# Performance work log

Hardware: AMD Instinct MI355X
Metric: run time of the kernel (lower is better)

Reference implementation:

```python
import jax, jax.numpy as jnp
import numpy as np

N = 100000   # nodes
E = 1600000  # edges (avg degree 16)
IDIM = 128
HDIM = 128   # heads=1, so heads*hdim == hdim
ODIM = 40
L = 4        # num_layers


def setup_inputs() -> dict:
    key = jax.random.key(0)
    ks = jax.random.split(key, 12)
    s = 0.05  # init scale
    inp = {
        "x": jax.random.normal(ks[0], (N, IDIM), jnp.float32),
        "edge_index": jax.random.randint(ks[1], (2, E), 0, N, jnp.int32),
        # input projection (idim -> hdim)
        "lin_W": jax.random.normal(ks[2], (IDIM, HDIM), jnp.float32) * s,
        "lin_b": jnp.zeros((HDIM,), jnp.float32),
        # stacked per-layer transformer-conv weights (heads=1)
        "Wq": jax.random.normal(ks[3], (L, HDIM, HDIM), jnp.float32) * s,
        "bq": jnp.zeros((L, HDIM), jnp.float32),
        "Wk": jax.random.normal(ks[4], (L, HDIM, HDIM), jnp.float32) * s,
        "bk": jnp.zeros((L, HDIM), jnp.float32),
        "Wv": jax.random.normal(ks[5], (L, HDIM, HDIM), jnp.float32) * s,
        "bv": jnp.zeros((L, HDIM), jnp.float32),
        "Ws": jax.random.normal(ks[6], (L, HDIM, HDIM), jnp.float32) * s,  # lin_skip
        "bs": jnp.zeros((L, HDIM), jnp.float32),
        # output classifier (hdim -> odim)
        "fc_W": jax.random.normal(ks[7], (HDIM, ODIM), jnp.float32) * s,
        "fc_b": jnp.zeros((ODIM,), jnp.float32),
    }
    return inp


def reference(x, edge_index, lin_W, lin_b, Wq, bq, Wk, bk, Wv, bv, Ws, bs, fc_W, fc_b):
    src = edge_index[0]  # x_j (message source)
    dst = edge_index[1]  # x_i (aggregation target / softmax segment)
    scale = 1.0 / np.sqrt(HDIM).astype(np.float32)

    h = x @ lin_W + lin_b  # [N, HDIM]
    for l in range(L):
        q = h @ Wq[l] + bq[l]  # [N, C]
        k = h @ Wk[l] + bk[l]
        v = h @ Wv[l] + bv[l]
        # per-edge attention logits: (W3 x_i) . (W4 x_j) / sqrt(d)
        logits = jnp.sum(q[dst] * k[src], axis=-1) * scale  # [E]
        # segment softmax over incoming edges of each dst node
        m = jax.ops.segment_max(logits, dst, num_segments=N)
        m = jnp.where(jnp.isfinite(m), m, 0.0)  # guard isolated nodes
        e = jnp.exp(logits - m[dst])
        den = jax.ops.segment_sum(e, dst, num_segments=N)
        alpha = e / jnp.where(den > 0, den, 1.0)[dst]  # [E]
        # weighted scatter-add aggregation
        agg = jax.ops.segment_sum(alpha[:, None] * v[src], dst, num_segments=N)  # [N, C]
        # root/skip connection (root_weight=True, beta=False)
        h = agg + (h @ Ws[l] + bs[l])
        if l < L - 1:
            h = jax.nn.elu(h)
    return jax.nn.log_softmax(h @ fc_W + fc_b, axis=1)  # [N, ODIM]
```

## Files before the change

### kernel.cpp

```cpp
#include <hip/hip_runtime.h>
#include <hip/hip_bf16.h>
#include <math.h>


#define HD 128
#define ODIM 40
#define LDSA 136
#define QK_SCALE_L2E 0.1275174368437563f
#define FIXED_M 8.0f

#define BKT_CAP 8192

typedef __attribute__((ext_vector_type(8))) short short8;
typedef __attribute__((ext_vector_type(4))) float f4v;
typedef __attribute__((ext_vector_type(2))) float f2v;
typedef __attribute__((ext_vector_type(4))) unsigned short us4;
typedef __attribute__((ext_vector_type(8))) unsigned short us8;
typedef __attribute__((ext_vector_type(4))) int i4v;
typedef long long ll64;

static __device__ __forceinline__ float b2f(unsigned short u) {
  return __uint_as_float(((unsigned)u) << 16);
}
static __device__ __forceinline__ unsigned short f2b(float f) {
  __hip_bfloat16 h = __float2bfloat16(f);
  return __builtin_bit_cast(unsigned short, h);
}


__global__ __launch_bounds__(256) void k_zero(int* __restrict__ p, int n) {
  int i = blockIdx.x * 256 + threadIdx.x;
  if (i < n) p[i] = 0;
}

__global__ __launch_bounds__(256) void k_bin(const int* __restrict__ src, const int* __restrict__ dst,
                                             int E, int NB, int* __restrict__ bucket_wp,
                                             unsigned int* __restrict__ staged) {
  __shared__ int cnt[512];
  __shared__ int lbase[512];
  int t = threadIdx.x;
  int e0 = blockIdx.x * 8192;
  for (int b = t; b < NB; b += 256) cnt[b] = 0;
  __syncthreads();
#pragma unroll
  for (int i = 0; i < 32; ++i) {
    int e = e0 + i * 256 + t;
    if (e < E) atomicAdd(&cnt[dst[e] >> 8], 1);
  }
  __syncthreads();
  for (int b = t; b < NB; b += 256) {
    int c = cnt[b];
    lbase[b] = (c > 0) ? atomicAdd(&bucket_wp[b], c) : 0;
    cnt[b] = 0;
  }
  __syncthreads();
#pragma unroll
  for (int i = 0; i < 32; ++i) {
    int e = e0 + i * 256 + t;
    if (e < E) {
      int d = dst[e];
      int b = d >> 8;
      int off = atomicAdd(&cnt[b], 1);
      int idx = lbase[b] + off;
      if (idx < BKT_CAP) {
        unsigned rec = (unsigned)src[e] | ((unsigned)(d & 255) << 17);
        staged[(size_t)b * BKT_CAP + idx] = rec;
      }
    }
  }
}

__global__ __launch_bounds__(512) void k_bscan(const int* __restrict__ bucket_wp, int NB, int E, int N,
                                               int* __restrict__ bucket_base, int* __restrict__ rowptr) {
  __shared__ int buf[512];
  int t = threadIdx.x;
  int v = (t < NB) ? bucket_wp[t] : 0;
  buf[t] = v;
  __syncthreads();
  for (int off = 1; off < 512; off <<= 1) {
    int x = (t >= off) ? buf[t - off] : 0;
    __syncthreads();
    buf[t] += x;
    __syncthreads();
  }
  if (t < NB) bucket_base[t] = buf[t] - v;
  if (t == 0) rowptr[N] = E;
}

__global__ __launch_bounds__(256) void k_csr(const unsigned int* __restrict__ staged,
                                             const int* __restrict__ bucket_wp,
                                             const int* __restrict__ bucket_base,
                                             int N, int* __restrict__ rowptr, int* __restrict__ colsrc) {
  __shared__ unsigned int srec[BKT_CAP];
  __shared__ int ncnt[256];
  __shared__ int noff[256];
  int b = blockIdx.x, t = threadIdx.x;
  int cnt = bucket_wp[b];
  if (cnt > BKT_CAP) cnt = BKT_CAP;
  int base = bucket_base[b];
  const unsigned int* gsrc = staged + (size_t)b * BKT_CAP;
  for (int i = t; i < cnt; i += 256) srec[i] = gsrc[i];
  ncnt[t] = 0;
  __syncthreads();
  for (int i = t; i < cnt; i += 256) atomicAdd(&ncnt[srec[i] >> 17], 1);
  __syncthreads();
  int v = ncnt[t];
  noff[t] = v;
  __syncthreads();
  for (int off = 1; off < 256; off <<= 1) {
    int x = (t >= off) ? noff[t - off] : 0;
    __syncthreads();
    noff[t] += x;
    __syncthreads();
  }
  int excl = noff[t] - v;
  int node = (b << 8) + t;
  if (node < N) rowptr[node] = base + excl;
  ncnt[t] = excl;
  __syncthreads();
  for (int i = t; i < cnt; i += 256) {
    unsigned rec = srec[i];
    int dl = rec >> 17;
    int pos = atomicAdd(&ncnt[dl], 1);
    colsrc[base + pos] = (int)(rec & 0x1FFFFu);
  }
}


#define PACK_FC   278528
#define PACK_TOT  284672

__global__ __launch_bounds__(256) void k_pack(const float* __restrict__ linW,
                                              const float* __restrict__ Wq, const float* __restrict__ Wk,
                                              const float* __restrict__ Wv, const float* __restrict__ Ws,
                                              const float* __restrict__ fcW,
                                              unsigned short* __restrict__ Wp) {
  int idx = blockIdx.x * 256 + threadIdx.x;
  float val;
  if (idx < 16384) {
    int n = idx >> 7, kk = idx & 127;
    val = linW[kk * 128 + n];
  } else if (idx < PACK_FC) {
    int t = idx - 16384;
    int l = t >> 16, r = t & 65535;
    int n_pos = r >> 7, k_pos = r & 127;
    int which = n_pos >> 7;
    int nn = n_pos & 127;
    int kk = 16 * (k_pos & 7) + (k_pos >> 3);
    const float* W = (which == 0) ? Wq : (which == 1) ? Wk : (which == 2) ? Wv : Ws;
    val = W[(size_t)l * 16384 + kk * 128 + nn];
  } else if (idx < PACK_TOT) {
    int t = idx - PACK_FC;
    int n = t >> 7, k_pos = t & 127;
    int kk = 16 * (k_pos & 7) + (k_pos >> 3);
    val = (n < ODIM) ? fcW[kk * ODIM + n] : 0.f;
  } else {
    return;
  }
  Wp[idx] = f2b(val);
}


__global__ __launch_bounds__(256) void k_gemm_lin(const float* __restrict__ x,
                                                  const unsigned short* __restrict__ wl,
                                                  const float* __restrict__ bias,
                                                  unsigned short* __restrict__ hb, int N) {
  __shared__ unsigned short As[32 * LDSA];
  int t = threadIdx.x;
  int rowbase = blockIdx.x * 32;
#pragma unroll
  for (int i = 0; i < 2; ++i) {
    int c = t + i * 256;
    int r = c >> 4, c8 = c & 15;
    int gr = rowbase + r;
    if (gr >= N) gr = N - 1;
    const float4* xp = (const float4*)(x + (size_t)gr * 128 + c8 * 8);
    float4 u0 = xp[0], u1 = xp[1];
    us8 o;
    o[0] = f2b(u0.x); o[1] = f2b(u0.y); o[2] = f2b(u0.z); o[3] = f2b(u0.w);
    o[4] = f2b(u1.x); o[5] = f2b(u1.y); o[6] = f2b(u1.z); o[7] = f2b(u1.w);
    *(us8*)(As + r * LDSA + c8 * 8) = o;
  }
  __syncthreads();

  int lane = t & 63, w = t >> 6;
  int rh = (w & 1) * 16;
  int ch = (w >> 1) * 64;
  int lm = lane & 15, lq = lane >> 4;

  short8 a[4];
#pragma unroll
  for (int ks = 0; ks < 4; ++ks)
    a[ks] = *(const short8*)(As + (rh + lm) * LDSA + ks * 32 + lq * 8);

  f4v acc[4];
#pragma unroll
  for (int ct = 0; ct < 4; ++ct) acc[ct] = (f4v){0.f, 0.f, 0.f, 0.f};

#pragma unroll
  for (int ct = 0; ct < 4; ++ct) {
    const short8* bp = (const short8*)(wl + ((size_t)(ch + ct * 16 + lm)) * 128 + lq * 8);
    short8 b0 = bp[0], b1 = bp[4], b2 = bp[8], b3 = bp[12];
    acc[ct] = __builtin_amdgcn_mfma_f32_16x16x32_bf16(a[0], b0, acc[ct], 0, 0, 0);
    acc[ct] = __builtin_amdgcn_mfma_f32_16x16x32_bf16(a[1], b1, acc[ct], 0, 0, 0);
    acc[ct] = __builtin_amdgcn_mfma_f32_16x16x32_bf16(a[2], b2, acc[ct], 0, 0, 0);
    acc[ct] = __builtin_amdgcn_mfma_f32_16x16x32_bf16(a[3], b3, acc[ct], 0, 0, 0);
  }

  float bv[4];
#pragma unroll
  for (int ct = 0; ct < 4; ++ct) bv[ct] = bias[ch + ct * 16 + lm];

#pragma unroll
  for (int r = 0; r < 4; ++r) {
    int row = rowbase + rh + lq * 4 + r;
    if (row < N) {
      us4 ov;
#pragma unroll
      for (int ct = 0; ct < 4; ++ct) ov[ct] = f2b(acc[ct][r] + bv[ct]);
      *(us4*)(hb + (size_t)row * 128 + lm * 8 + (w >> 1) * 4) = ov;
    }
  }
}


__global__ __launch_bounds__(256, 3) void k_gemm_qkvs(const unsigned short* __restrict__ hb,
                                                      const unsigned short* __restrict__ wl,
                                                      const float* __restrict__ bq, const float* __restrict__ bk,
                                                      const float* __restrict__ bv, const float* __restrict__ bs,
                                                      unsigned char* __restrict__ q8, unsigned char* __restrict__ k8,
                                                      unsigned char* __restrict__ v8, unsigned short* __restrict__ s,
                                                      int N) {
  __shared__ unsigned short As[32 * LDSA];
  int t = threadIdx.x;
  int rowbase = blockIdx.x * 32;
#pragma unroll
  for (int i = 0; i < 2; ++i) {
    int c = t + i * 256;
    int r = c >> 4, c8 = c & 15;
    int gr = rowbase + r;
    if (gr >= N) gr = N - 1;
    *(us8*)(As + r * LDSA + c8 * 8) = *(const us8*)(hb + (size_t)gr * 128 + c8 * 8);
  }
  __syncthreads();

  int lane = t & 63, w = t >> 6;
  int lm = lane & 15, lq = lane >> 4;

  short8 a[2][4];
#pragma unroll
  for (int rt = 0; rt < 2; ++rt)
#pragma unroll
    for (int ks = 0; ks < 4; ++ks)
      a[rt][ks] = *(const short8*)(As + (rt * 16 + lm) * LDSA + ks * 32 + lq * 8);

  f4v acc[2][8];
#pragma unroll
  for (int rt = 0; rt < 2; ++rt)
#pragma unroll
    for (int ct = 0; ct < 8; ++ct) acc[rt][ct] = (f4v){0.f, 0.f, 0.f, 0.f};

  const unsigned short* wb = wl + (size_t)w * 16384;
#pragma unroll
  for (int ct = 0; ct < 8; ++ct) {
    const short8* bp = (const short8*)(wb + (size_t)(ct * 16 + lm) * 128 + lq * 8);
    short8 b0 = bp[0], b1 = bp[4], b2 = bp[8], b3 = bp[12];
#pragma unroll
    for (int rt = 0; rt < 2; ++rt) {
      acc[rt][ct] = __builtin_amdgcn_mfma_f32_16x16x32_bf16(a[rt][0], b0, acc[rt][ct], 0, 0, 0);
      acc[rt][ct] = __builtin_amdgcn_mfma_f32_16x16x32_bf16(a[rt][1], b1, acc[rt][ct], 0, 0, 0);
      acc[rt][ct] = __builtin_amdgcn_mfma_f32_16x16x32_bf16(a[rt][2], b2, acc[rt][ct], 0, 0, 0);
      acc[rt][ct] = __builtin_amdgcn_mfma_f32_16x16x32_bf16(a[rt][3], b3, acc[rt][ct], 0, 0, 0);
    }
  }

  const float* bsel = (w == 0) ? bq : (w == 1) ? bk : (w == 2) ? bv : bs;
  float bias[8];
#pragma unroll
  for (int ct = 0; ct < 8; ++ct) bias[ct] = bsel[ct * 16 + lm];

#pragma unroll
  for (int rt = 0; rt < 2; ++rt) {
#pragma unroll
    for (int r = 0; r < 4; ++r) {
      int row = rowbase + rt * 16 + lq * 4 + r;
      if (row >= N) continue;
      float vals[8];
#pragma unroll
      for (int ct = 0; ct < 8; ++ct) vals[ct] = acc[rt][ct][r] + bias[ct];
      if (w <= 2) {
        float sc = (w == 1) ? QK_SCALE_L2E : 1.0f;
        unsigned u0 = __builtin_amdgcn_cvt_pk_fp8_f32(vals[0] * sc, vals[1] * sc, 0, false);
        u0 = __builtin_amdgcn_cvt_pk_fp8_f32(vals[2] * sc, vals[3] * sc, u0, true);
        unsigned u1 = __builtin_amdgcn_cvt_pk_fp8_f32(vals[4] * sc, vals[5] * sc, 0, false);
        u1 = __builtin_amdgcn_cvt_pk_fp8_f32(vals[6] * sc, vals[7] * sc, u1, true);
        uint2 kw; kw.x = u0; kw.y = u1;
        unsigned char* outp = (w == 0) ? q8 : (w == 1) ? k8 : v8;
        *(uint2*)(outp + (size_t)row * 128 + lm * 8) = kw;
      } else {
        us8 ov;
#pragma unroll
        for (int ct = 0; ct < 8; ++ct) ov[ct] = f2b(vals[ct]);
        *(us8*)(s + (size_t)row * 128 + lm * 8) = ov;
      }
    }
  }
}


__global__ __launch_bounds__(256, 8) void k_attn_mfma(const unsigned char* __restrict__ q8,
                                                      const unsigned char* __restrict__ kb8,
                                                      const unsigned char* __restrict__ v8,
                                                      const unsigned short* __restrict__ s,
                                                      const int* __restrict__ rowptr, const int* __restrict__ colsrc,
                                                      unsigned short* __restrict__ hb, int n, int do_elu) {
  int wid = blockIdx.x * 4 + (threadIdx.x >> 6);
  if (wid >= n) return;
  int lane = threadIdx.x & 63;
  int lm = lane & 15;
  int lq = lane >> 4;

  const unsigned char* qrow = q8 + (size_t)wid * 128;
  ll64 Bf[4];
#pragma unroll
  for (int km = 0; km < 4; ++km)
    Bf[km] = *(const ll64*)(qrow + km * 32 + lq * 8);

  int e0 = rowptr[wid], e1 = rowptr[wid + 1];

  float Sp = 0.f;
  f2v av[4];
#pragma unroll
  for (int i = 0; i < 4; ++i) av[i] = (f2v){0.f, 0.f};

  for (int ebase = e0; ebase < e1; ebase += 16) {
    int ja = colsrc[min(ebase + lm, e1 - 1)];
    const unsigned char* krow = kb8 + (size_t)ja * 128;
    ll64 Af[4];
#pragma unroll
    for (int km = 0; km < 4; ++km)
      Af[km] = *(const ll64*)(krow + km * 32 + lq * 8);

    uint2 vw[4];
#pragma unroll
    for (int r = 0; r < 4; ++r) {
      int jv = __shfl(ja, lq * 4 + r, 64);
      vw[r] = *(const uint2*)(v8 + (size_t)jv * 128 + lm * 8);
    }

    f4v c = (f4v){0.f, 0.f, 0.f, 0.f};
#pragma unroll
    for (int km = 0; km < 4; ++km)
      c = __builtin_amdgcn_mfma_f32_16x16x32_fp8_fp8(Af[km], Bf[km], c, 0, 0, 0);

    float w[4];
#pragma unroll
    for (int r = 0; r < 4; ++r)
      w[r] = (ebase + lq * 4 + r < e1) ? exp2f(c[r] - FIXED_M) : 0.f;
    Sp += (w[0] + w[1]) + (w[2] + w[3]);
#pragma unroll
    for (int r = 0; r < 4; ++r) {
      f2v p01 = __builtin_amdgcn_cvt_pk_f32_fp8(vw[r].x, false);
      f2v p23 = __builtin_amdgcn_cvt_pk_f32_fp8(vw[r].x, true);
      f2v p45 = __builtin_amdgcn_cvt_pk_f32_fp8(vw[r].y, false);
      f2v p67 = __builtin_amdgcn_cvt_pk_f32_fp8(vw[r].y, true);
      f2v wv = (f2v){w[r], w[r]};
      av[0] += p01 * wv;
      av[1] += p23 * wv;
      av[2] += p45 * wv;
      av[3] += p67 * wv;
    }
  }

#pragma unroll
  for (int off = 16; off <= 32; off <<= 1) {
    Sp += __shfl_xor(Sp, off, 64);
#pragma unroll
    for (int i = 0; i < 4; ++i) {
      av[i][0] += __shfl_xor(av[i][0], off, 64);
      av[i][1] += __shfl_xor(av[i][1], off, 64);
    }
  }

  if (lq == 0) {
    int d0 = lm * 8;
    float inv = (Sp > 0.f) ? 1.f / Sp : 0.f;
    us8 sk = *(const us8*)(s + (size_t)wid * 128 + d0);
    us8 ov;
#pragma unroll
    for (int i = 0; i < 8; ++i) {
      float x = av[i / 2][i & 1] * inv + b2f(sk[i]);
      if (do_elu) x = (x > 0.f) ? x : (__expf(x) - 1.f);
      ov[i] = f2b(x);
    }
    *(us8*)(hb + (size_t)wid * 128 + d0) = ov;
  }
}


__global__ __launch_bounds__(256) void k_fc_mfma(const unsigned short* __restrict__ hb,
                                                 const unsigned short* __restrict__ fcp,
                                                 const float* __restrict__ fcb,
                                                 float* __restrict__ out, int N) {
  __shared__ unsigned short As[64 * LDSA];
  int t = threadIdx.x;
  int rowbase = blockIdx.x * 64;
#pragma unroll
  for (int i = 0; i < 4; ++i) {
    int c = t + i * 256;
    int r = c >> 4, c8 = c & 15;
    int gr = rowbase + r;
    if (gr >= N) gr = N - 1;
    us8 val = *(const us8*)(hb + (size_t)gr * 128 + c8 * 8);
    *(us8*)(As + r * LDSA + c8 * 8) = val;
  }
  __syncthreads();

  int lane = t & 63, w = t >> 6;
  int rh = w * 16;
  int lm = lane & 15, lq = lane >> 4;

  short8 a[4];
#pragma unroll
  for (int ks = 0; ks < 4; ++ks)
    a[ks] = *(const short8*)(As + (rh + lm) * LDSA + ks * 32 + lq * 8);

  f4v acc[3];
#pragma unroll
  for (int ct = 0; ct < 3; ++ct) acc[ct] = (f4v){0.f, 0.f, 0.f, 0.f};

#pragma unroll
  for (int ct = 0; ct < 3; ++ct) {
    const short8* bp = (const short8*)(fcp + ((size_t)(ct * 16 + lm)) * 128 + lq * 8);
    short8 b0 = bp[0], b1 = bp[4], b2 = bp[8], b3 = bp[12];
    acc[ct] = __builtin_amdgcn_mfma_f32_16x16x32_bf16(a[0], b0, acc[ct], 0, 0, 0);
    acc[ct] = __builtin_amdgcn_mfma_f32_16x16x32_bf16(a[1], b1, acc[ct], 0, 0, 0);
    acc[ct] = __builtin_amdgcn_mfma_f32_16x16x32_bf16(a[2], b2, acc[ct], 0, 0, 0);
    acc[ct] = __builtin_amdgcn_mfma_f32_16x16x32_bf16(a[3], b3, acc[ct], 0, 0, 0);
  }

  float bias[3];
#pragma unroll
  for (int ct = 0; ct < 3; ++ct) {
    int c = ct * 16 + lm;
    bias[ct] = (c < ODIM) ? fcb[c] : 0.f;
  }

#pragma unroll
  for (int r = 0; r < 4; ++r) {
    float v0 = acc[0][r] + bias[0];
    float v1 = acc[1][r] + bias[1];
    float v2 = (32 + lm < ODIM) ? (acc[2][r] + bias[2]) : -INFINITY;
    float m = fmaxf(fmaxf(v0, v1), v2);
#pragma unroll
    for (int off = 1; off <= 8; off <<= 1) m = fmaxf(m, __shfl_xor(m, off, 64));
    float sum = __expf(v0 - m) + __expf(v1 - m) + ((32 + lm < ODIM) ? __expf(v2 - m) : 0.f);
#pragma unroll
    for (int off = 1; off <= 8; off <<= 1) sum += __shfl_xor(sum, off, 64);
    float lse = m + logf(sum);
    int row = rowbase + rh + lq * 4 + r;
    if (row < N) {
      float* orow = out + (size_t)row * ODIM;
      orow[lm] = v0 - lse;
      orow[16 + lm] = v1 - lse;
      if (32 + lm < ODIM) orow[32 + lm] = v2 - lse;
    }
  }
}


extern "C" void kernel_launch(void* const* d_in, const int* in_sizes, int n_in,
                              void* d_out, int out_size, void* d_ws, size_t ws_size,
                              hipStream_t stream) {
  const float* x    = (const float*)d_in[0];
  const int*   ei   = (const int*)d_in[1];
  const float* linW = (const float*)d_in[2];
  const float* linb = (const float*)d_in[3];
  const float* Wq   = (const float*)d_in[4];
  const float* bq   = (const float*)d_in[5];
  const float* Wk   = (const float*)d_in[6];
  const float* bk   = (const float*)d_in[7];
  const float* Wv   = (const float*)d_in[8];
  const float* bv   = (const float*)d_in[9];
  const float* Wsk  = (const float*)d_in[10];
  const float* bsk  = (const float*)d_in[11];
  const float* fcW  = (const float*)d_in[12];
  const float* fcb  = (const float*)d_in[13];
  float* out = (float*)d_out;

  const int N = in_sizes[0] / HD;
  const int E = in_sizes[1] / 2;
  const int* srcv = ei;
  const int* dstv = ei + E;
  const int NB = (N + 255) >> 8;

  size_t off = 0;
  char* base = (char*)d_ws;
  auto carve = [&](size_t bytes) -> void* {
    void* p = base + off;
    off = (off + bytes + 255) & ~(size_t)255;
    return p;
  };
  unsigned short* Wp = (unsigned short*)carve((size_t)PACK_TOT * 2);
  unsigned short* hb = (unsigned short*)carve((size_t)N * HD * 2);
  unsigned char*  q8 = (unsigned char*)carve((size_t)N * HD);
  unsigned char*  k8 = (unsigned char*)carve((size_t)N * HD);
  unsigned char*  v8 = (unsigned char*)carve((size_t)N * HD);
  unsigned short* sbuf = (unsigned short*)carve((size_t)N * HD * 2);
  int* rowptr = (int*)carve((size_t)(N + 1) * 4);
  int* colsrc = (int*)carve((size_t)E * 4);
  int* bucket_wp   = (int*)carve((size_t)NB * 4);
  int* bucket_base = (int*)carve((size_t)NB * 4);
  unsigned int* staged = (unsigned int*)carve((size_t)NB * BKT_CAP * 4);
  (void)ws_size; (void)n_in; (void)out_size;

  dim3 blk(256);
  int gx = (N + 31) / 32;
  int wb = (N + 3) / 4;

  k_zero<<<(NB + 255) / 256, blk, 0, stream>>>(bucket_wp, NB);
  k_bin<<<(E + 8191) / 8192, blk, 0, stream>>>(srcv, dstv, E, NB, bucket_wp, staged);
  k_bscan<<<1, 512, 0, stream>>>(bucket_wp, NB, E, N, bucket_base, rowptr);
  k_csr<<<NB, blk, 0, stream>>>(staged, bucket_wp, bucket_base, N, rowptr, colsrc);

  k_pack<<<(PACK_TOT + 255) / 256, blk, 0, stream>>>(linW, Wq, Wk, Wv, Wsk, fcW, Wp);

  k_gemm_lin<<<gx, blk, 0, stream>>>(x, Wp, linb, hb, N);

  for (int l = 0; l < 4; ++l) {
    const unsigned short* wl = Wp + 16384 + (size_t)l * 65536;
    k_gemm_qkvs<<<gx, blk, 0, stream>>>(hb, wl, bq + l * HD, bk + l * HD, bv + l * HD, bsk + l * HD,
                                        q8, k8, v8, sbuf, N);
    k_attn_mfma<<<wb, blk, 0, stream>>>(q8, k8, v8, sbuf, rowptr, colsrc, hb, N, (l < 3) ? 1 : 0);
  }

  k_fc_mfma<<<(N + 63) / 64, blk, 0, stream>>>(hb, Wp + PACK_FC, fcb, out, N);
}
```

Before: 798.7 us.

## Interleave K and V rows and process 32 edges per attention iteration

K and V fp8 rows are stored interleaved in a single 256-byte-per-node buffer, so a neighbour's K and V sit in adjacent memory and gathers have better locality. The attention loop now handles two 16-edge groups per iteration, issuing twice as many independent gathers and MFMAs to hide memory latency. Occupancy hint drops from 8 to 6 blocks per CU because the unrolled loop needs more registers. Nodes with fewer than 32 edges waste some lanes on masked work.

```diff
diff --git a/kernel.cpp b/kernel.cpp
--- a/kernel.cpp
+++ b/kernel.cpp
@@ -16,7 +16,6 @@
 typedef __attribute__((ext_vector_type(2))) float f2v;
 typedef __attribute__((ext_vector_type(4))) unsigned short us4;
 typedef __attribute__((ext_vector_type(8))) unsigned short us8;
-typedef __attribute__((ext_vector_type(4))) int i4v;
 typedef long long ll64;
 
 static __device__ __forceinline__ float b2f(unsigned short u) {
@@ -228,8 +227,8 @@
                                                       const unsigned short* __restrict__ wl,
                                                       const float* __restrict__ bq, const float* __restrict__ bk,
                                                       const float* __restrict__ bv, const float* __restrict__ bs,
-                                                      unsigned char* __restrict__ q8, unsigned char* __restrict__ k8,
-                                                      unsigned char* __restrict__ v8, unsigned short* __restrict__ s,
+                                                      unsigned char* __restrict__ q8, unsigned char* __restrict__ kv,
+                                                      unsigned short* __restrict__ s,
                                                       int N) {
   __shared__ unsigned short As[32 * LDSA];
   int t = threadIdx.x;
@@ -295,8 +294,10 @@
         unsigned u1 = __builtin_amdgcn_cvt_pk_fp8_f32(vals[4] * sc, vals[5] * sc, 0, false);
         u1 = __builtin_amdgcn_cvt_pk_fp8_f32(vals[6] * sc, vals[7] * sc, u1, true);
         uint2 kw; kw.x = u0; kw.y = u1;
-        unsigned char* outp = (w == 0) ? q8 : (w == 1) ? k8 : v8;
-        *(uint2*)(outp + (size_t)row * 128 + lm * 8) = kw;
+        unsigned char* outp = (w == 0) ? (q8 + (size_t)row * 128 + lm * 8)
+                            : (w == 1) ? (kv + (size_t)row * 256 + lm * 8)
+                                       : (kv + (size_t)row * 256 + 128 + lm * 8);
+        *(uint2*)outp = kw;
       } else {
         us8 ov;
 #pragma unroll
@@ -308,9 +309,8 @@
 }
 
 
-__global__ __launch_bounds__(256, 8) void k_attn_mfma(const unsigned char* __restrict__ q8,
-                                                      const unsigned char* __restrict__ kb8,
-                                                      const unsigned char* __restrict__ v8,
+__global__ __launch_bounds__(256, 6) void k_attn_mfma(const unsigned char* __restrict__ q8,
+                                                      const unsigned char* __restrict__ kv,
                                                       const unsigned short* __restrict__ s,
                                                       const int* __restrict__ rowptr, const int* __restrict__ colsrc,
                                                       unsigned short* __restrict__ hb, int n, int do_elu) {
@@ -333,42 +333,54 @@
 #pragma unroll
   for (int i = 0; i < 4; ++i) av[i] = (f2v){0.f, 0.f};
 
-  for (int ebase = e0; ebase < e1; ebase += 16) {
-    int ja = colsrc[min(ebase + lm, e1 - 1)];
-    const unsigned char* krow = kb8 + (size_t)ja * 128;
-    ll64 Af[4];
-#pragma unroll
-    for (int km = 0; km < 4; ++km)
-      Af[km] = *(const ll64*)(krow + km * 32 + lq * 8);
-
-    uint2 vw[4];
+  for (int ebase = e0; ebase < e1; ebase += 32) {
+    int ja0 = colsrc[min(ebase + lm, e1 - 1)];
+    int ja1 = colsrc[min(ebase + 16 + lm, e1 - 1)];
+    const unsigned char* kr0 = kv + (size_t)ja0 * 256;
+    const unsigned char* kr1 = kv + (size_t)ja1 * 256;
+    ll64 Af0[4], Af1[4];
+#pragma unroll
+    for (int km = 0; km < 4; ++km) {
+      Af0[km] = *(const ll64*)(kr0 + km * 32 + lq * 8);
+      Af1[km] = *(const ll64*)(kr1 + km * 32 + lq * 8);
+    }
+
+    uint2 vw0[4], vw1[4];
 #pragma unroll
     for (int r = 0; r < 4; ++r) {
-      int jv = __shfl(ja, lq * 4 + r, 64);
-      vw[r] = *(const uint2*)(v8 + (size_t)jv * 128 + lm * 8);
-    }
-
-    f4v c = (f4v){0.f, 0.f, 0.f, 0.f};
-#pragma unroll
-    for (int km = 0; km < 4; ++km)
-      c = __builtin_amdgcn_mfma_f32_16x16x32_fp8_fp8(Af[km], Bf[km], c, 0, 0, 0);
-
-    float w[4];
-#pragma unroll
-    for (int r = 0; r < 4; ++r)
-      w[r] = (ebase + lq * 4 + r < e1) ? exp2f(c[r] - FIXED_M) : 0.f;
-    Sp += (w[0] + w[1]) + (w[2] + w[3]);
+      int jv0 = __shfl(ja0, lq * 4 + r, 64);
+      int jv1 = __shfl(ja1, lq * 4 + r, 64);
+      vw0[r] = *(const uint2*)(kv + (size_t)jv0 * 256 + 128 + lm * 8);
+      vw1[r] = *(const uint2*)(kv + (size_t)jv1 * 256 + 128 + lm * 8);
+    }
+
+    f4v c0 = (f4v){0.f, 0.f, 0.f, 0.f};
+    f4v c1 = (f4v){0.f, 0.f, 0.f, 0.f};
+#pragma unroll
+    for (int km = 0; km < 4; ++km) {
+      c0 = __builtin_amdgcn_mfma_f32_16x16x32_fp8_fp8(Af0[km], Bf[km], c0, 0, 0, 0);
+      c1 = __builtin_amdgcn_mfma_f32_16x16x32_fp8_fp8(Af1[km], Bf[km], c1, 0, 0, 0);
+    }
+
+    float w0[4], w1[4];
 #pragma unroll
     for (int r = 0; r < 4; ++r) {
-      f2v p01 = __builtin_amdgcn_cvt_pk_f32_fp8(vw[r].x, false);
-      f2v p23 = __builtin_amdgcn_cvt_pk_f32_fp8(vw[r].x, true);
-      f2v p45 = __builtin_amdgcn_cvt_pk_f32_fp8(vw[r].y, false);
-      f2v p67 = __builtin_amdgcn_cvt_pk_f32_fp8(vw[r].y, true);
-      f2v wv = (f2v){w[r], w[r]};
-      av[0] += p01 * wv;
-      av[1] += p23 * wv;
-      av[2] += p45 * wv;
-      av[3] += p67 * wv;
+      w0[r] = (ebase + lq * 4 + r < e1) ? exp2f(c0[r] - FIXED_M) : 0.f;
+      w1[r] = (ebase + 16 + lq * 4 + r < e1) ? exp2f(c1[r] - FIXED_M) : 0.f;
+    }
+    Sp += ((w0[0] + w0[1]) + (w0[2] + w0[3])) + ((w1[0] + w1[1]) + (w1[2] + w1[3]));
+#pragma unroll
+    for (int r = 0; r < 4; ++r) {
+      f2v wv0 = (f2v){w0[r], w0[r]};
+      av[0] += __builtin_amdgcn_cvt_pk_f32_fp8(vw0[r].x, false) * wv0;
+      av[1] += __builtin_amdgcn_cvt_pk_f32_fp8(vw0[r].x, true) * wv0;
+      av[2] += __builtin_amdgcn_cvt_pk_f32_fp8(vw0[r].y, false) * wv0;
+      av[3] += __builtin_amdgcn_cvt_pk_f32_fp8(vw0[r].y, true) * wv0;
+      f2v wv1 = (f2v){w1[r], w1[r]};
+      av[0] += __builtin_amdgcn_cvt_pk_f32_fp8(vw1[r].x, false) * wv1;
+      av[1] += __builtin_amdgcn_cvt_pk_f32_fp8(vw1[r].x, true) * wv1;
+      av[2] += __builtin_amdgcn_cvt_pk_f32_fp8(vw1[r].y, false) * wv1;
+      av[3] += __builtin_amdgcn_cvt_pk_f32_fp8(vw1[r].y, true) * wv1;
     }
   }
 
@@ -504,8 +516,7 @@
   unsigned short* Wp = (unsigned short*)carve((size_t)PACK_TOT * 2);
   unsigned short* hb = (unsigned short*)carve((size_t)N * HD * 2);
   unsigned char*  q8 = (unsigned char*)carve((size_t)N * HD);
-  unsigned char*  k8 = (unsigned char*)carve((size_t)N * HD);
-  unsigned char*  v8 = (unsigned char*)carve((size_t)N * HD);
+  unsigned char*  kvb = (unsigned char*)carve((size_t)N * HD * 2);
   unsigned short* sbuf = (unsigned short*)carve((size_t)N * HD * 2);
   int* rowptr = (int*)carve((size_t)(N + 1) * 4);
   int* colsrc = (int*)carve((size_t)E * 4);
@@ -530,8 +541,8 @@
   for (int l = 0; l < 4; ++l) {
     const unsigned short* wl = Wp + 16384 + (size_t)l * 65536;
     k_gemm_qkvs<<<gx, blk, 0, stream>>>(hb, wl, bq + l * HD, bk + l * HD, bv + l * HD, bsk + l * HD,
-                                        q8, k8, v8, sbuf, N);
-    k_attn_mfma<<<wb, blk, 0, stream>>>(q8, k8, v8, sbuf, rowptr, colsrc, hb, N, (l < 3) ? 1 : 0);
+                                        q8, kvb, sbuf, N);
+    k_attn_mfma<<<wb, blk, 0, stream>>>(q8, kvb, sbuf, rowptr, colsrc, hb, N, (l < 3) ? 1 : 0);
   }
 
   k_fc_mfma<<<(N + 63) / 64, blk, 0, stream>>>(hb, Wp + PACK_FC, fcb, out, N);
```

New measurement: 844.0 us. 5.7% more time.
